# Performance work log

Hardware: AMD Instinct MI355X
Metric: run time of the kernel (lower is better)

## Reference

```python
import jax, jax.numpy as jnp
import numpy as np

H = 512   # hidden_dim (args.hidden_dim)
D = 128   # data_dim (tones)
N = 64    # num_sequences
T = 512   # max_length


def setup_inputs() -> dict:
    key = jax.random.key(0)
    k1, k2, k3, k4 = jax.random.split(key, 4)
    # Transition matrix: rows on the simplex, biased toward identity (Dirichlet(0.9*I + 0.1) prior).
    probs_x = jax.nn.softmax(jax.random.normal(k1, (H, H)) + 2.0 * jnp.eye(H), axis=-1)
    # Bernoulli emission probabilities (Beta(0.1, 0.9) prior -> values in (0,1), skewed low).
    probs_y = jax.nn.sigmoid(jax.random.normal(k2, (H, D)) - 1.0)
    # Observed binary tone sequences.
    sequences = (jax.random.uniform(k3, (N, T, D)) < 0.3).astype(jnp.float32)
    # Valid lengths in [T//2, T].
    lengths = jnp.sort(jax.random.randint(k4, (N,), T // 2, T + 1)).astype(jnp.int32)
    return {"sequences": sequences, "lengths": lengths, "probs_x": probs_x, "probs_y": probs_y}


def reference(sequences, lengths, probs_x, probs_y):
    """Enumerated-HMM forward algorithm: log p(sequences[n, :lengths[n]]) per sequence.

    Matches Pyro's parallel enumeration of x_t ~ Categorical(probs_x[x_{t-1}]) starting
    from x = 0, with observations y_t ~ Bernoulli(probs_y[x_t]) masked by t < lengths.
    """
    N_, T_, D_ = sequences.shape
    log_px = jnp.log(probs_x)        # [H, H]
    log_py = jnp.log(probs_y)        # [H, D]
    log_1mpy = jnp.log1p(-probs_y)   # [H, D]

    # Bernoulli emission log-likelihood summed over the tones plate: [N, T, H]
    emit = (jnp.einsum('ntd,hd->nth', sequences, log_py)
            + jnp.einsum('ntd,hd->nth', 1.0 - sequences, log_1mpy))

    # t = 0: initial hidden state drawn from probs_x[0] (x starts at 0).
    log_alpha0 = log_px[0][None, :] + emit[:, 0]   # [N, H] (lengths >= 1 so t=0 is unmasked)

    emits = jnp.moveaxis(emit[:, 1:], 1, 0)        # [T-1, N, H]
    ts = jnp.arange(1, T_)

    def step(log_alpha, inp):
        emit_t, t = inp
        # logsumexp over previous state: [N, H_prev] + [H_prev, H_next] -> [N, H_next]
        new = jax.nn.logsumexp(log_alpha[:, :, None] + log_px[None, :, :], axis=1) + emit_t
        mask = (t < lengths)[:, None]
        return jnp.where(mask, new, log_alpha), None

    log_alpha, _ = jax.lax.scan(step, log_alpha0, (emits, ts))
    return jax.nn.logsumexp(log_alpha, axis=-1)    # [N] per-sequence log-likelihood
```

## Files before the change

kernel.cpp:

```cpp
#include <hip/hip_runtime.h>
#include <stdint.h>

#define Hn 512
#define Dn 128
#define Nn 64
#define Tn 512
#define NT (Nn*Tn)

typedef unsigned int uint;
typedef unsigned short ushort;
typedef unsigned long long u64;

typedef __attribute__((ext_vector_type(4))) float f32x4;
typedef __attribute__((ext_vector_type(8))) int i32x8;
typedef __attribute__((ext_vector_type(8))) short short8;

#define WG_BARRIER() asm volatile("s_waitcnt lgkmcnt(0)\n\ts_barrier" ::: "memory")


__device__ inline float bf2f(ushort u) { union { uint i; float f; } v; v.i = uint(u) << 16; return v.f; }
__device__ inline float ubits(uint u) { union { uint i; float f; } v; v.i = u; return v.f; }
__device__ inline ushort f2bf(float f) {
  union { uint i; float f; } v; v.f = f;
  uint u = v.i;
  uint r = (u + 0x7FFFu + ((u >> 16) & 1u)) >> 16;
  return ushort(r);
}
__device__ inline float fp8val(uint b) {
  uint e = (b >> 3) & 15u, m = b & 7u;
  return e ? ldexpf((float)(8u + m), (int)e - 10) : ldexpf((float)m, -9);
}
__device__ inline u64 pack8fp8(const float* v, float qs) {
  int lo = 0, hi = 0;
  lo = __builtin_amdgcn_cvt_pk_fp8_f32(v[0] * qs, v[1] * qs, lo, false);
  lo = __builtin_amdgcn_cvt_pk_fp8_f32(v[2] * qs, v[3] * qs, lo, true);
  hi = __builtin_amdgcn_cvt_pk_fp8_f32(v[4] * qs, v[5] * qs, hi, false);
  hi = __builtin_amdgcn_cvt_pk_fp8_f32(v[6] * qs, v[7] * qs, hi, true);
  return (u64)(uint)lo | ((u64)(uint)hi << 32);
}
__device__ inline int permcol(int c) {
  return (c & ~63) | ((c & 12) << 2) | ((c & 48) >> 2) | (c & 3);
}

__global__ void k_prep(const float* __restrict__ py, ushort* __restrict__ wmatb,
                       float* __restrict__ bias) {
  int h = blockIdx.x, d = threadIdx.x;
  float p = py[h * Dn + d];
  float lp = logf(p), l1 = log1pf(-p);
  wmatb[h * Dn + d] = f2bf(lp - l1);
  float v = l1;
  for (int o = 1; o < 64; o <<= 1) v += __shfl_xor(v, o, 64);
  __shared__ float s2[2];
  if ((threadIdx.x & 63) == 0) s2[threadIdx.x >> 6] = v;
  __syncthreads();
  if (threadIdx.x == 0) bias[h] = s2[0] + s2[1];
}

__global__ __launch_bounds__(1024) void k_cs(const float* __restrict__ px, float* __restrict__ cs,
                                             float* __restrict__ rcsg, float* __restrict__ px0sp) {
  __shared__ float pm[512];
  int t = threadIdx.x;
  int j = t & 511, half = t >> 9;
  float m = 0.f;
  const float* p = px + (size_t)half * 256 * Hn + j;
#pragma unroll 8
  for (int k = 0; k < 256; k++) m = fmaxf(m, p[(size_t)k * Hn]);
  if (half) pm[j] = m;
  __syncthreads();
  if (!half) {
    m = fmaxf(m, pm[j]);
    float c = 448.0f / m;
    cs[j] = c;
    rcsg[j] = m * (1.0f / 448.0f);
    px0sp[permcol(j)] = px[j] * c;
  }
}

__global__ __launch_bounds__(256) void k_pq(const float* __restrict__ px, const float* __restrict__ cs,
                                            u64* __restrict__ pq) {
  __shared__ float ksl[512][17];
  int ntg = blockIdx.x;
  int t = threadIdx.x;
  for (int i = 0; i < 8; i++) {
    int q = i * 256 + t;
    int row = q >> 2, c4 = q & 3;
    float4 v = *(const float4*)(px + (size_t)row * Hn + ntg * 16 + c4 * 4);
    ksl[row][c4 * 4 + 0] = v.x; ksl[row][c4 * 4 + 1] = v.y;
    ksl[row][c4 * 4 + 2] = v.z; ksl[row][c4 * 4 + 3] = v.w;
  }
  __syncthreads();
  int kb = t >> 6, lane = t & 63, qa = lane >> 4, c15 = lane & 15;
  float csv = cs[ntg * 16 + c15];
  int kbase = kb * 128 + (qa >> 1) * 64 + (qa & 1) * 8;
  size_t base = ((size_t)(((ntg >> 2) * 16 + kb * 4 + (ntg & 3)) * 64 + lane)) * 4;
#pragma unroll
  for (int d = 0; d < 4; d++) {
    float vv[8];
#pragma unroll
    for (int b = 0; b < 8; b++) {
      int jj = d * 8 + b;
      int kk = kbase + (((jj >> 2) & 3) << 4) + ((jj >> 4) << 2) + (jj & 3);
      vv[b] = ksl[kk][c15];
    }
    pq[base + d] = pack8fp8(vv, csv);
  }
}

__global__ __launch_bounds__(256, 1) void k_emit3(
    const float* __restrict__ A, const ushort* __restrict__ wmatb,
    const float* __restrict__ bias, const float* __restrict__ rcsg,
    ushort* __restrict__ eb, float* __restrict__ rm) {
  __shared__ ushort Bs[512][136];
  __shared__ ushort As[64][136];
  __shared__ float biasL[512];
  __shared__ float rcsL[512];
  int t = threadIdx.x;
  int r0 = blockIdx.x * 64;
  for (int i = 0; i < 32; i++) {
    int q = i * 256 + t, row = q >> 4, c = q & 15;
    *(uint4*)&Bs[row][c * 8] = *(const uint4*)(wmatb + row * 128 + c * 8);
  }
  for (int i = 0; i < 8; i++) {
    int q = i * 256 + t, row = q >> 5, c4 = q & 31;
    float4 v = *(const float4*)(A + (size_t)(r0 + row) * Dn + c4 * 4);
    ushort4 u4 = {f2bf(v.x), f2bf(v.y), f2bf(v.z), f2bf(v.w)};
    *(ushort4*)&As[row][c4 * 4] = u4;
  }
  biasL[t] = bias[t]; biasL[t + 256] = bias[t + 256];
  rcsL[t] = rcsg[t];  rcsL[t + 256] = rcsg[t + 256];
  __syncthreads();

  const int w = t >> 6, lane = t & 63, l15 = lane & 15, g4 = lane >> 4;
  short8 afr[4];
#pragma unroll
  for (int kt = 0; kt < 4; kt++)
    afr[kt] = *(const short8*)&As[w * 16 + l15][kt * 32 + g4 * 8];

  f32x4 acc[32];
#pragma unroll
  for (int nt = 0; nt < 32; nt++) {
    f32x4 a = {0.f, 0.f, 0.f, 0.f};
#pragma unroll
    for (int kt = 0; kt < 4; kt++) {
      short8 bfr = *(const short8*)&Bs[nt * 16 + l15][kt * 32 + g4 * 8];
      a = __builtin_amdgcn_mfma_f32_16x16x32_bf16(afr[kt], bfr, a, 0, 0, 0);
    }
    acc[nt] = a;
  }
  float mrow[4] = {-1e30f, -1e30f, -1e30f, -1e30f};
#pragma unroll
  for (int nt = 0; nt < 32; nt++) {
    float bv = biasL[nt * 16 + l15];
#pragma unroll
    for (int r = 0; r < 4; r++) {
      float v = acc[nt][r] + bv;
      acc[nt][r] = v;
      mrow[r] = fmaxf(mrow[r], v);
    }
  }
#pragma unroll
  for (int o = 1; o < 16; o <<= 1) {
    mrow[0] = fmaxf(mrow[0], __shfl_xor(mrow[0], o, 64));
    mrow[1] = fmaxf(mrow[1], __shfl_xor(mrow[1], o, 64));
    mrow[2] = fmaxf(mrow[2], __shfl_xor(mrow[2], o, 64));
    mrow[3] = fmaxf(mrow[3], __shfl_xor(mrow[3], o, 64));
  }
  if (l15 == 0) {
#pragma unroll
    for (int r = 0; r < 4; r++) rm[(size_t)(r0 + w * 16 + g4 * 4 + r)] = mrow[r];
  }
  ushort* ebase = eb + (size_t)(r0 + w * 16 + g4 * 4) * Hn;
#pragma unroll
  for (int nt = 0; nt < 32; nt++) {
    int colp = (nt >> 2) * 64 + (l15 >> 2) * 16 + (nt & 3) * 4 + (l15 & 3);
    float rc = rcsL[nt * 16 + l15];
#pragma unroll
    for (int r = 0; r < 4; r++) {
      float e = __expf(acc[nt][r] - mrow[r]) * rc;
      ebase[(size_t)r * Hn + colp] = f2bf(e);
    }
  }
}

__global__ __launch_bounds__(512, 2) void k_rec9(
    const ushort* __restrict__ eb, const float* __restrict__ rm,
    const u64* __restrict__ pq, const float* __restrict__ px0sp,
    const int* __restrict__ lens, float* __restrict__ outp) {
  const int grp = blockIdx.x;
  const int t = threadIdx.x;
  const int w = t >> 6;
  const int lane = t & 63, qg = lane >> 4, l15 = lane & 15;

  __shared__ uint BfI[16 * 132];
  __shared__ float sredM[16][12];
  __shared__ float rmsL[16];
  __shared__ int lenl[16];

  i32x8 PRv[16];
  {
    const uint4* pqv = (const uint4*)pq;
#pragma unroll
    for (int f = 0; f < 16; f++) {
      uint4 p0 = pqv[((size_t)(w * 16 + f) * 64 + lane) * 2 + 0];
      uint4 p1 = pqv[((size_t)(w * 16 + f) * 64 + lane) * 2 + 1];
      i32x8 v = {(int)p0.x, (int)p0.y, (int)p0.z, (int)p0.w,
                 (int)p1.x, (int)p1.y, (int)p1.z, (int)p1.w};
      PRv[f] = v;
    }
  }

  if (t < 16) lenl[t] = lens[grp * 16 + t];
  const size_t seqstride = (size_t)Tn * Hn;
  const ushort* myrow = eb + (size_t)(grp * 16 + l15) * seqstride + w * 64 + qg * 16;
  uint* myslot = &BfI[l15 * 132 + (w * 4 + qg) * 4];

  float4 uv0, uv1, uv2, uv3;
  {
    uint4 e0 = *(const uint4*)myrow;
    uint4 e1 = *(const uint4*)(myrow + 8);
    float4 p0 = *(const float4*)(px0sp + w * 64 + qg * 16 + 0);
    float4 p1 = *(const float4*)(px0sp + w * 64 + qg * 16 + 4);
    float4 p2 = *(const float4*)(px0sp + w * 64 + qg * 16 + 8);
    float4 p3 = *(const float4*)(px0sp + w * 64 + qg * 16 + 12);
    uv0.x = p0.x * ubits(e0.x << 16);  uv0.y = p0.y * ubits(e0.x & 0xffff0000u);
    uv0.z = p0.z * ubits(e0.y << 16);  uv0.w = p0.w * ubits(e0.y & 0xffff0000u);
    uv1.x = p1.x * ubits(e0.z << 16);  uv1.y = p1.y * ubits(e0.z & 0xffff0000u);
    uv1.z = p1.z * ubits(e0.w << 16);  uv1.w = p1.w * ubits(e0.w & 0xffff0000u);
    uv2.x = p2.x * ubits(e1.x << 16);  uv2.y = p2.y * ubits(e1.x & 0xffff0000u);
    uv2.z = p2.z * ubits(e1.y << 16);  uv2.w = p2.w * ubits(e1.y & 0xffff0000u);
    uv3.x = p3.x * ubits(e1.z << 16);  uv3.y = p3.y * ubits(e1.z & 0xffff0000u);
    uv3.z = p3.z * ubits(e1.w << 16);  uv3.w = p3.w * ubits(e1.w & 0xffff0000u);
    float m01 = fmaxf(fmaxf(fmaxf(uv0.x, uv0.y), fmaxf(uv0.z, uv0.w)),
                      fmaxf(fmaxf(uv1.x, uv1.y), fmaxf(uv1.z, uv1.w)));
    float m23 = fmaxf(fmaxf(fmaxf(uv2.x, uv2.y), fmaxf(uv2.z, uv2.w)),
                      fmaxf(fmaxf(uv3.x, uv3.y), fmaxf(uv3.z, uv3.w)));
    float mxv = fmaxf(m01, m23);
    mxv = fmaxf(mxv, __shfl_xor(mxv, 16, 64));
    mxv = fmaxf(mxv, __shfl_xor(mxv, 32, 64));
    if (qg == 0) sredM[l15][w] = mxv;
  }
  WG_BARRIER();
  const int t_end = lenl[15];
  const int lenq = lenl[l15];
  float L2acc;
  u64 myf0, myf1;

  {
    float4 g0 = *(const float4*)&sredM[l15][0];
    float4 g1 = *(const float4*)&sredM[l15][4];
    float gm = fmaxf(fmaxf(fmaxf(g0.x, g0.y), fmaxf(g0.z, g0.w)),
                     fmaxf(fmaxf(g1.x, g1.y), fmaxf(g1.z, g1.w)));
    L2acc = __log2f(gm);
    float qs = 448.0f * __builtin_amdgcn_rcpf(gm);
    float v0[8] = {uv0.x, uv0.y, uv0.z, uv0.w, uv1.x, uv1.y, uv1.z, uv1.w};
    float v1[8] = {uv2.x, uv2.y, uv2.z, uv2.w, uv3.x, uv3.y, uv3.z, uv3.w};
    myf0 = pack8fp8(v0, qs);
    myf1 = pack8fp8(v1, qs);
    *(uint4*)myslot = (uint4){(uint)myf0, (uint)(myf0 >> 32), (uint)myf1, (uint)(myf1 >> 32)};
  }

  const ushort* epp = myrow + Hn;
  uint4 bpA = *(const uint4*)epp;
  uint4 bpB = *(const uint4*)(epp + 8);
  epp += Hn;

  for (int ts = 1; ts < t_end; ts++) {
    WG_BARRIER();
    uint4 bqA = *(const uint4*)epp;
    uint4 bqB = *(const uint4*)(epp + 8);
    epp += Hn;

    f32x4 ac0 = {0.f, 0.f, 0.f, 0.f}, ac1 = {0.f, 0.f, 0.f, 0.f};
    f32x4 ac2 = {0.f, 0.f, 0.f, 0.f}, ac3 = {0.f, 0.f, 0.f, 0.f};
#pragma unroll
    for (int kb = 0; kb < 4; kb++) {
      const uint* bp_ = &BfI[l15 * 132 + (kb * 8 + qg * 2) * 4];
      uint4 b0 = *(const uint4*)bp_;
      uint4 b1 = *(const uint4*)(bp_ + 4);
      i32x8 bf = {(int)b0.x, (int)b0.y, (int)b0.z, (int)b0.w,
                  (int)b1.x, (int)b1.y, (int)b1.z, (int)b1.w};
      ac0 = __builtin_amdgcn_mfma_scale_f32_16x16x128_f8f6f4(
          PRv[kb * 4 + 0], bf, ac0, 0, 0, 0, 0x7F7F7F7F, 0, 0x7F7F7F7F);
      ac1 = __builtin_amdgcn_mfma_scale_f32_16x16x128_f8f6f4(
          PRv[kb * 4 + 1], bf, ac1, 0, 0, 0, 0x7F7F7F7F, 0, 0x7F7F7F7F);
      ac2 = __builtin_amdgcn_mfma_scale_f32_16x16x128_f8f6f4(
          PRv[kb * 4 + 2], bf, ac2, 0, 0, 0, 0x7F7F7F7F, 0, 0x7F7F7F7F);
      ac3 = __builtin_amdgcn_mfma_scale_f32_16x16x128_f8f6f4(
          PRv[kb * 4 + 3], bf, ac3, 0, 0, 0, 0x7F7F7F7F, 0, 0x7F7F7F7F);
    }

    {
      uv0.x = ac0[0] * ubits(bpA.x << 16);  uv0.y = ac0[1] * ubits(bpA.x & 0xffff0000u);
      uv0.z = ac0[2] * ubits(bpA.y << 16);  uv0.w = ac0[3] * ubits(bpA.y & 0xffff0000u);
      uv1.x = ac1[0] * ubits(bpA.z << 16);  uv1.y = ac1[1] * ubits(bpA.z & 0xffff0000u);
      uv1.z = ac1[2] * ubits(bpA.w << 16);  uv1.w = ac1[3] * ubits(bpA.w & 0xffff0000u);
      uv2.x = ac2[0] * ubits(bpB.x << 16);  uv2.y = ac2[1] * ubits(bpB.x & 0xffff0000u);
      uv2.z = ac2[2] * ubits(bpB.y << 16);  uv2.w = ac2[3] * ubits(bpB.y & 0xffff0000u);
      uv3.x = ac3[0] * ubits(bpB.z << 16);  uv3.y = ac3[1] * ubits(bpB.z & 0xffff0000u);
      uv3.z = ac3[2] * ubits(bpB.w << 16);  uv3.w = ac3[3] * ubits(bpB.w & 0xffff0000u);
      float m01 = fmaxf(fmaxf(fmaxf(uv0.x, uv0.y), fmaxf(uv0.z, uv0.w)),
                        fmaxf(fmaxf(uv1.x, uv1.y), fmaxf(uv1.z, uv1.w)));
      float m23 = fmaxf(fmaxf(fmaxf(uv2.x, uv2.y), fmaxf(uv2.z, uv2.w)),
                        fmaxf(fmaxf(uv3.x, uv3.y), fmaxf(uv3.z, uv3.w)));
      float mxv = fmaxf(m01, m23);
      mxv = fmaxf(mxv, __shfl_xor(mxv, 16, 64));
      mxv = fmaxf(mxv, __shfl_xor(mxv, 32, 64));
      if (qg == 0) sredM[l15][w] = mxv;
    }
    WG_BARRIER();

    if (ts < lenq) {
      float4 g0 = *(const float4*)&sredM[l15][0];
      float4 g1 = *(const float4*)&sredM[l15][4];
      float gm = fmaxf(fmaxf(fmaxf(g0.x, g0.y), fmaxf(g0.z, g0.w)),
                       fmaxf(fmaxf(g1.x, g1.y), fmaxf(g1.z, g1.w)));
      L2acc += __log2f(gm);
      float qs = 448.0f * __builtin_amdgcn_rcpf(gm);
      float v0[8] = {uv0.x, uv0.y, uv0.z, uv0.w, uv1.x, uv1.y, uv1.z, uv1.w};
      float v1[8] = {uv2.x, uv2.y, uv2.z, uv2.w, uv3.x, uv3.y, uv3.z, uv3.w};
      myf0 = pack8fp8(v0, qs);
      myf1 = pack8fp8(v1, qs);
      *(uint4*)myslot = (uint4){(uint)myf0, (uint)(myf0 >> 32), (uint)myf1, (uint)(myf1 >> 32)};
    }
    bpA = bqA; bpB = bqB;
  }

  WG_BARRIER();
  {
    float ps = 0.f;
#pragma unroll
    for (int j = 0; j < 8; j++) {
      ps += fp8val((uint)(myf0 >> (8 * j)) & 0xffu);
      ps += fp8val((uint)(myf1 >> (8 * j)) & 0xffu);
    }
    ps += __shfl_xor(ps, 16, 64);
    ps += __shfl_xor(ps, 32, 64);
    if (qg == 0) sredM[l15][w] = ps;
  }
  {
    int sq = 2 * w + (lane >> 5), tl = lane & 31;
    const float* rp = rm + (size_t)(grp * 16 + sq) * Tn;
    int ls = lenl[sq];
    float rs = 0.f;
#pragma unroll
    for (int k = 0; k < 16; k++) {
      int idx = tl + 32 * k;
      float v = rp[idx];
      rs += (idx < ls) ? v : 0.f;
    }
#pragma unroll
    for (int o = 1; o < 32; o <<= 1) rs += __shfl_xor(rs, o, 64);
    if ((lane & 31) == 0) rmsL[sq] = rs;
  }
  __syncthreads();
  if (t < 16) {
    float4 s0 = *(const float4*)&sredM[t][0];
    float4 s1 = *(const float4*)&sredM[t][4];
    float Ss = (s0.x + s0.y) + (s0.z + s0.w) + (s1.x + s1.y) + (s1.z + s1.w);
    outp[grp * 16 + t] = 0.6931471805599453f * L2acc - (float)lenq * 6.104793232414985f
                         + logf(Ss) + rmsL[t];
  }
}

extern "C" void kernel_launch(void* const* d_in, const int* in_sizes, int n_in,
                              void* d_out, int out_size, void* d_ws, size_t ws_size,
                              hipStream_t stream) {
  const float* seq = (const float*)d_in[0];
  const int* lens = (const int*)d_in[1];
  const float* px = (const float*)d_in[2];
  const float* py = (const float*)d_in[3];
  char* ws = (char*)d_ws;
  ushort* emitb = (ushort*)(ws + 0x0000000);
  float* rm     = (float*)(ws + 0x2000000);
  ushort* wmatb = (ushort*)(ws + 0x2020000);
  float* bias   = (float*)(ws + 0x2060000);
  float* cs     = (float*)(ws + 0x2061000);
  float* rcsg   = (float*)(ws + 0x2062000);
  float* px0sp  = (float*)(ws + 0x2063000);
  u64* pq       = (u64*)(ws + 0x2070000);
  float* outp   = (float*)d_out;

  hipLaunchKernelGGL(k_prep, dim3(512), dim3(128), 0, stream, py, wmatb, bias);
  hipLaunchKernelGGL(k_cs, dim3(1), dim3(1024), 0, stream, px, cs, rcsg, px0sp);
  hipLaunchKernelGGL(k_pq, dim3(32), dim3(256), 0, stream, px, cs, pq);
  hipLaunchKernelGGL(k_emit3, dim3(NT / 64), dim3(256), 0, stream, seq, wmatb, bias, rcsg, emitb, rm);
  hipLaunchKernelGGL(k_rec9, dim3(4), dim3(512), 0, stream, emitb, rm, pq, px0sp, lens, outp);
}
```

Baseline: 662.6 us.

## Fuse column-scale into pq kernel, chunk emit B tile, retune recurrence loop

```diff
diff --git a/kernel.cpp b/kernel.cpp
--- a/kernel.cpp
+++ b/kernel.cpp
@@ -56,29 +56,12 @@
   if (threadIdx.x == 0) bias[h] = s2[0] + s2[1];
 }
 
-__global__ __launch_bounds__(1024) void k_cs(const float* __restrict__ px, float* __restrict__ cs,
-                                             float* __restrict__ rcsg, float* __restrict__ px0sp) {
-  __shared__ float pm[512];
-  int t = threadIdx.x;
-  int j = t & 511, half = t >> 9;
-  float m = 0.f;
-  const float* p = px + (size_t)half * 256 * Hn + j;
-#pragma unroll 8
-  for (int k = 0; k < 256; k++) m = fmaxf(m, p[(size_t)k * Hn]);
-  if (half) pm[j] = m;
-  __syncthreads();
-  if (!half) {
-    m = fmaxf(m, pm[j]);
-    float c = 448.0f / m;
-    cs[j] = c;
-    rcsg[j] = m * (1.0f / 448.0f);
-    px0sp[permcol(j)] = px[j] * c;
-  }
-}
-
-__global__ __launch_bounds__(256) void k_pq(const float* __restrict__ px, const float* __restrict__ cs,
+__global__ __launch_bounds__(256) void k_pq(const float* __restrict__ px,
+                                            float* __restrict__ rcsg, float* __restrict__ px0sp,
                                             u64* __restrict__ pq) {
   __shared__ float ksl[512][17];
+  __shared__ float pm[16][17];
+  __shared__ float csL[16];
   int ntg = blockIdx.x;
   int t = threadIdx.x;
   for (int i = 0; i < 8; i++) {
@@ -89,8 +72,26 @@
     ksl[row][c4 * 4 + 2] = v.z; ksl[row][c4 * 4 + 3] = v.w;
   }
   __syncthreads();
+  {
+    int c = t & 15, ch = t >> 4;
+    float m = 0.f;
+#pragma unroll
+    for (int r = 0; r < 32; r++) m = fmaxf(m, ksl[ch * 32 + r][c]);
+    pm[ch][c] = m;
+  }
+  __syncthreads();
+  if (t < 16) {
+    float m = pm[0][t];
+#pragma unroll
+    for (int i = 1; i < 16; i++) m = fmaxf(m, pm[i][t]);
+    float c = 448.0f / m;
+    csL[t] = c;
+    rcsg[ntg * 16 + t] = m * (1.0f / 448.0f);
+    px0sp[permcol(ntg * 16 + t)] = px[ntg * 16 + t] * c;
+  }
+  __syncthreads();
   int kb = t >> 6, lane = t & 63, qa = lane >> 4, c15 = lane & 15;
-  float csv = cs[ntg * 16 + c15];
+  float csv = csL[c15];
   int kbase = kb * 128 + (qa >> 1) * 64 + (qa & 1) * 8;
   size_t base = ((size_t)(((ntg >> 2) * 16 + kb * 4 + (ntg & 3)) * 64 + lane)) * 4;
 #pragma unroll
@@ -106,20 +107,16 @@
   }
 }
 
-__global__ __launch_bounds__(256, 1) void k_emit3(
+__global__ __launch_bounds__(256, 2) void k_emit3(
     const float* __restrict__ A, const ushort* __restrict__ wmatb,
     const float* __restrict__ bias, const float* __restrict__ rcsg,
     ushort* __restrict__ eb, float* __restrict__ rm) {
-  __shared__ ushort Bs[512][136];
+  __shared__ ushort Bs[128][136];
   __shared__ ushort As[64][136];
   __shared__ float biasL[512];
   __shared__ float rcsL[512];
   int t = threadIdx.x;
   int r0 = blockIdx.x * 64;
-  for (int i = 0; i < 32; i++) {
-    int q = i * 256 + t, row = q >> 4, c = q & 15;
-    *(uint4*)&Bs[row][c * 8] = *(const uint4*)(wmatb + row * 128 + c * 8);
-  }
   for (int i = 0; i < 8; i++) {
     int q = i * 256 + t, row = q >> 5, c4 = q & 31;
     float4 v = *(const float4*)(A + (size_t)(r0 + row) * Dn + c4 * 4);
@@ -137,15 +134,24 @@
     afr[kt] = *(const short8*)&As[w * 16 + l15][kt * 32 + g4 * 8];
 
   f32x4 acc[32];
-#pragma unroll
-  for (int nt = 0; nt < 32; nt++) {
-    f32x4 a = {0.f, 0.f, 0.f, 0.f};
-#pragma unroll
-    for (int kt = 0; kt < 4; kt++) {
-      short8 bfr = *(const short8*)&Bs[nt * 16 + l15][kt * 32 + g4 * 8];
-      a = __builtin_amdgcn_mfma_f32_16x16x32_bf16(afr[kt], bfr, a, 0, 0, 0);
-    }
-    acc[nt] = a;
+  for (int cc = 0; cc < 4; cc++) {
+    __syncthreads();
+    for (int i = 0; i < 8; i++) {
+      int q = i * 256 + t, row = q >> 4, c = q & 15;
+      *(uint4*)&Bs[row][c * 8] = *(const uint4*)(wmatb + (cc * 128 + row) * 128 + c * 8);
+    }
+    __syncthreads();
+#pragma unroll
+    for (int n8 = 0; n8 < 8; n8++) {
+      int nt = cc * 8 + n8;
+      f32x4 a = {0.f, 0.f, 0.f, 0.f};
+#pragma unroll
+      for (int kt = 0; kt < 4; kt++) {
+        short8 bfr = *(const short8*)&Bs[n8 * 16 + l15][kt * 32 + g4 * 8];
+        a = __builtin_amdgcn_mfma_f32_16x16x32_bf16(afr[kt], bfr, a, 0, 0, 0);
+      }
+      acc[nt] = a;
+    }
   }
   float mrow[4] = {-1e30f, -1e30f, -1e30f, -1e30f};
 #pragma unroll
@@ -191,7 +197,7 @@
   const int w = t >> 6;
   const int lane = t & 63, qg = lane >> 4, l15 = lane & 15;
 
-  __shared__ uint BfI[16 * 132];
+  __shared__ uint4 BfI[32][16];
   __shared__ float sredM[16][12];
   __shared__ float rmsL[16];
   __shared__ int lenl[16];
@@ -212,7 +218,7 @@
   if (t < 16) lenl[t] = lens[grp * 16 + t];
   const size_t seqstride = (size_t)Tn * Hn;
   const ushort* myrow = eb + (size_t)(grp * 16 + l15) * seqstride + w * 64 + qg * 16;
-  uint* myslot = &BfI[l15 * 132 + (w * 4 + qg) * 4];
+  uint4* myslot = &BfI[w * 4 + qg][l15];
 
   float4 uv0, uv1, uv2, uv3;
   {
@@ -256,7 +262,7 @@
     float v1[8] = {uv2.x, uv2.y, uv2.z, uv2.w, uv3.x, uv3.y, uv3.z, uv3.w};
     myf0 = pack8fp8(v0, qs);
     myf1 = pack8fp8(v1, qs);
-    *(uint4*)myslot = (uint4){(uint)myf0, (uint)(myf0 >> 32), (uint)myf1, (uint)(myf1 >> 32)};
+    *myslot = (uint4){(uint)myf0, (uint)(myf0 >> 32), (uint)myf1, (uint)(myf1 >> 32)};
   }
 
   const ushort* epp = myrow + Hn;
@@ -266,17 +272,14 @@
 
   for (int ts = 1; ts < t_end; ts++) {
     WG_BARRIER();
-    uint4 bqA = *(const uint4*)epp;
-    uint4 bqB = *(const uint4*)(epp + 8);
-    epp += Hn;
 
     f32x4 ac0 = {0.f, 0.f, 0.f, 0.f}, ac1 = {0.f, 0.f, 0.f, 0.f};
     f32x4 ac2 = {0.f, 0.f, 0.f, 0.f}, ac3 = {0.f, 0.f, 0.f, 0.f};
+    __builtin_amdgcn_s_setprio(1);
 #pragma unroll
     for (int kb = 0; kb < 4; kb++) {
-      const uint* bp_ = &BfI[l15 * 132 + (kb * 8 + qg * 2) * 4];
-      uint4 b0 = *(const uint4*)bp_;
-      uint4 b1 = *(const uint4*)(bp_ + 4);
+      uint4 b0 = BfI[kb * 8 + qg * 2 + 0][l15];
+      uint4 b1 = BfI[kb * 8 + qg * 2 + 1][l15];
       i32x8 bf = {(int)b0.x, (int)b0.y, (int)b0.z, (int)b0.w,
                   (int)b1.x, (int)b1.y, (int)b1.z, (int)b1.w};
       ac0 = __builtin_amdgcn_mfma_scale_f32_16x16x128_f8f6f4(
@@ -288,6 +291,11 @@
       ac3 = __builtin_amdgcn_mfma_scale_f32_16x16x128_f8f6f4(
           PRv[kb * 4 + 3], bf, ac3, 0, 0, 0, 0x7F7F7F7F, 0, 0x7F7F7F7F);
     }
+    __builtin_amdgcn_s_setprio(0);
+
+    uint4 bqA = *(const uint4*)epp;
+    uint4 bqB = *(const uint4*)(epp + 8);
+    epp += Hn;
 
     {
       uv0.x = ac0[0] * ubits(bpA.x << 16);  uv0.y = ac0[1] * ubits(bpA.x & 0xffff0000u);
@@ -320,7 +328,7 @@
       float v1[8] = {uv2.x, uv2.y, uv2.z, uv2.w, uv3.x, uv3.y, uv3.z, uv3.w};
       myf0 = pack8fp8(v0, qs);
       myf1 = pack8fp8(v1, qs);
-      *(uint4*)myslot = (uint4){(uint)myf0, (uint)(myf0 >> 32), (uint)myf1, (uint)(myf1 >> 32)};
+      *myslot = (uint4){(uint)myf0, (uint)(myf0 >> 32), (uint)myf1, (uint)(myf1 >> 32)};
     }
     bpA = bqA; bpB = bqB;
   }
@@ -374,15 +382,13 @@
   float* rm     = (float*)(ws + 0x2000000);
   ushort* wmatb = (ushort*)(ws + 0x2020000);
   float* bias   = (float*)(ws + 0x2060000);
-  float* cs     = (float*)(ws + 0x2061000);
   float* rcsg   = (float*)(ws + 0x2062000);
   float* px0sp  = (float*)(ws + 0x2063000);
   u64* pq       = (u64*)(ws + 0x2070000);
   float* outp   = (float*)d_out;
 
   hipLaunchKernelGGL(k_prep, dim3(512), dim3(128), 0, stream, py, wmatb, bias);
-  hipLaunchKernelGGL(k_cs, dim3(1), dim3(1024), 0, stream, px, cs, rcsg, px0sp);
-  hipLaunchKernelGGL(k_pq, dim3(32), dim3(256), 0, stream, px, cs, pq);
+  hipLaunchKernelGGL(k_pq, dim3(32), dim3(256), 0, stream, px, rcsg, px0sp, pq);
   hipLaunchKernelGGL(k_emit3, dim3(NT / 64), dim3(256), 0, stream, seq, wmatb, bias, rcsg, emitb, rm);
   hipLaunchKernelGGL(k_rec9, dim3(4), dim3(512), 0, stream, emitb, rm, pq, px0sp, lens, outp);
 }
```

Result: faster. 606.5 us (-8.5%).
